# Optimization experiments

Measured on AMD Instinct MI355X. Metric: run time of the kernel, lower is better.

The kernel has to match this reference:

```python
import jax, jax.numpy as jnp
import numpy as np

HID = 1024   # hidden_dim
H = 16       # num_head
D = 64       # head_dim
W = 64       # window_size (one-sided attention radius)


def setup_inputs() -> dict:
    key = jax.random.key(0)
    ks = jax.random.split(key, 10)
    B, S = 2, 4096
    s = 0.02
    X = jax.random.normal(ks[0], (B, S, HID), jnp.float32)
    mask = jnp.ones((B, S), jnp.float32)
    Wq = jax.random.normal(ks[1], (HID, H * D), jnp.float32) * s
    bq = jnp.zeros((H * D,), jnp.float32)
    Wk = jax.random.normal(ks[2], (HID, H * D), jnp.float32) * s
    bk = jnp.zeros((H * D,), jnp.float32)
    Wv = jax.random.normal(ks[3], (HID, H * D), jnp.float32) * s
    bv = jnp.zeros((H * D,), jnp.float32)
    Wo = jax.random.normal(ks[4], (H * D, HID), jnp.float32) * s
    bo = jnp.zeros((HID,), jnp.float32)
    return dict(X=X, mask=mask, Wq=Wq, bq=bq, Wk=Wk, bk=bk, Wv=Wv, bv=bv, Wo=Wo, bo=bo)


def _chunk3(T, nC):
    # T: [B,H,S,D] -> [B,H,nC,3W,D]: for chunk c, keys of chunks c-1, c, c+1 (zero-padded at ends)
    B, Hh, S, Dd = T.shape
    Tp = jnp.pad(T, ((0, 0), (0, 0), (W, W), (0, 0))).reshape(B, Hh, nC + 2, W, Dd)
    return jnp.concatenate([Tp[:, :, :-2], Tp[:, :, 1:-1], Tp[:, :, 2:]], axis=3)


def reference(X, mask, Wq, bq, Wk, bk, Wv, bv, Wo, bo):
    B, S0, _ = X.shape
    pad = W - S0 % W  # matches torch: always >= 1 (full window if divisible)
    Xp = jnp.pad(X, ((0, 0), (0, pad), (0, 0)))
    mp = jnp.pad(mask, ((0, 0), (0, pad)))  # padded keys masked out
    S = S0 + pad
    nC = S // W

    def proj(Wm, b):
        return (Xp @ Wm + b).reshape(B, S, H, D).transpose(0, 2, 1, 3)  # [B,H,S,D]

    Q, K, V = proj(Wq, bq), proj(Wk, bk), proj(Wv, bv)
    Qc = Q.reshape(B, H, nC, W, D)
    K3 = _chunk3(K, nC)
    V3 = _chunk3(V, nC)

    # banded scores: query i attends keys j with |i - j| <= W
    scores = jnp.einsum('bhcqd,bhckd->bhcqk', Qc, K3) / jnp.asarray(np.sqrt(D), jnp.float32)
    qi = jnp.arange(W)[:, None]
    kj = jnp.arange(3 * W)[None, :]
    band = (kj >= qi) & (kj <= qi + 2 * W)  # [W, 3W]
    m3 = jnp.pad(mp, ((0, 0), (W, W))).reshape(B, nC + 2, W)
    m3 = jnp.concatenate([m3[:, :-2], m3[:, 1:-1], m3[:, 2:]], axis=2)  # [B,nC,3W]
    valid = band[None, None, None, :, :] & (m3[:, None, :, None, :] > 0)
    scores = jnp.where(valid, scores, -1e9)
    A = jax.nn.softmax(scores, axis=-1)
    ctx = jnp.einsum('bhcqk,bhckd->bhcqd', A, V3).reshape(B, H, S, D)
    out = ctx.transpose(0, 2, 1, 3).reshape(B, S, H * D) @ Wo + bo
    return out[:, :S0]
```

## Files before the change

kernel.cpp:

```cpp
#include <hip/hip_runtime.h>

typedef unsigned short u16;
typedef unsigned int u32;
typedef __bf16 bf16x8 __attribute__((ext_vector_type(8)));
typedef u16 u16x8 __attribute__((ext_vector_type(8)));
typedef float floatx4 __attribute__((ext_vector_type(4)));

#define MFMA16(a, b, c) __builtin_amdgcn_mfma_f32_16x16x32_bf16((a), (b), (c), 0, 0, 0)

#define B_ 2
#define S0 4096
#define NH 16
#define HD 64
#define HID 1024

__device__ __forceinline__ float bf2f(u16 u) {
  union { u32 i; float f; } x; x.i = ((u32)u) << 16; return x.f;
}
__device__ __forceinline__ u16 f2bf(float f) {
  union { float f; u32 i; } x; x.f = f;
  u32 r = x.i + 0x7FFFu + ((x.i >> 16) & 1u);
  return (u16)(r >> 16);
}

__device__ __forceinline__ void glds16(const u16* g, u16* l) {
  __builtin_amdgcn_global_load_lds(
      (const __attribute__((address_space(1))) u32*)g,
      (__attribute__((address_space(3))) u32*)l, 16, 0, 0);
}

__global__ __launch_bounds__(256) void prep(
    const float* __restrict__ X, const float* __restrict__ mask,
    const float* __restrict__ Wq, const float* __restrict__ bq,
    const float* __restrict__ Wk, const float* __restrict__ bk,
    const float* __restrict__ Wv, const float* __restrict__ bv,
    const float* __restrict__ Wo, const float* __restrict__ bo,
    u16* __restrict__ cX, u16* __restrict__ cmask, u16* __restrict__ cb,
    u16* __restrict__ WqkvT, u16* __restrict__ WoT) {
  __shared__ u16 tile[64][66];
  int bid = blockIdx.x;
  if (bid < 4096) {
    int i = (bid * 256 + threadIdx.x) * 8;
    u16x8 v;
#pragma unroll
    for (int j = 0; j < 8; j++) v[j] = f2bf(X[i + j]);
    *(u16x8*)(cX + i) = v;
  } else if (bid < 4144) {
    int tid = (bid - 4096) * 256 + threadIdx.x;
    if (tid < B_ * S0) {
      cmask[tid] = f2bf(mask[tid]);
    } else {
      int j = tid - B_ * S0;
      int seg = j >> 10, idx = j & 1023;
      const float* src = (seg == 0) ? bq : (seg == 1) ? bk : (seg == 2) ? bv : bo;
      cb[seg * 1024 + idx] = f2bf(src[idx]);
    }
  } else {
    int idx = bid - 4144;
    int mat = idx >> 8;
    const float* src = (mat == 0) ? Wq : (mat == 1) ? Wk : (mat == 2) ? Wv : Wo;
    u16* dst = (mat < 3) ? (WqkvT + (size_t)mat * HID * HID) : WoT;
    int t0 = ((idx >> 4) & 15) * 64;
    int c0 = (idx & 15) * 64;
    int tx = threadIdx.x & 63, ty = threadIdx.x >> 6;
#pragma unroll
    for (int i = 0; i < 16; i++) {
      int r = i * 4 + ty;
      tile[r][tx] = f2bf(src[(size_t)(t0 + r) * HID + c0 + tx]);
    }
    __syncthreads();
#pragma unroll
    for (int i = 0; i < 16; i++) {
      int r = i * 4 + ty;
      dst[(size_t)(c0 + r) * HID + t0 + tx] = tile[tx][r];
    }
  }
}

template <int BN, int MODE>
__global__ __launch_bounds__(256) void gemm_bf16_tn(
    const u16* __restrict__ A, const u16* __restrict__ Bt,
    const u16* __restrict__ cb, void* __restrict__ outp, int K) {
  constexpr int NT = BN / 32;
  __shared__ alignas(16) u16 sA[128 * 64];
  __shared__ alignas(16) u16 sB[BN * 64];
  int t = threadIdx.x;
  int wave = t >> 6, lane = t & 63;
  int wm = wave >> 1, wn = wave & 1;
  int quad = lane >> 4, l16 = lane & 15;
  int tile_m = blockIdx.x * 128;
  int tile_n = blockIdx.y * BN;

  floatx4 acc[4][NT] = {};

  int row_l = lane >> 3;
  int col_l = ((lane & 7) ^ row_l) * 8;
  const u16* Ag = A + (size_t)(tile_m + wave * 8 + row_l) * K + col_l;
  const u16* Bg = Bt + (size_t)(tile_n + wave * 8 + row_l) * K + col_l;
  u16* lA = sA + wave * 8 * 64;
  u16* lB = sB + wave * 8 * 64;

  for (int k0 = 0; k0 < K; k0 += 64) {
    __syncthreads();
#pragma unroll
    for (int r = 0; r < 4; r++)
      glds16(Ag + (size_t)(r * 32) * K + k0, lA + r * 2048);
#pragma unroll
    for (int r = 0; r < BN / 32; r++)
      glds16(Bg + (size_t)(r * 32) * K + k0, lB + r * 2048);
    __syncthreads();

#pragma unroll
    for (int ks = 0; ks < 2; ks++) {
      bf16x8 af[4], bfr[NT];
#pragma unroll
      for (int mt = 0; mt < 4; mt++) {
        int row = wm * 64 + mt * 16 + l16;
        int p = (ks * 4 + quad) ^ (row & 7);
        af[mt] = *(const bf16x8*)(sA + row * 64 + p * 8);
      }
#pragma unroll
      for (int nt = 0; nt < NT; nt++) {
        int row = wn * (BN / 2) + nt * 16 + l16;
        int p = (ks * 4 + quad) ^ (row & 7);
        bfr[nt] = *(const bf16x8*)(sB + row * 64 + p * 8);
      }
#pragma unroll
      for (int mt = 0; mt < 4; mt++)
#pragma unroll
        for (int nt = 0; nt < NT; nt++)
          acc[mt][nt] = MFMA16(af[mt], bfr[nt], acc[mt][nt]);
    }
  }

  if (MODE == 0) {
    u16* op = (u16*)outp;
#pragma unroll
    for (int mt = 0; mt < 4; mt++) {
      int row0 = tile_m + wm * 64 + mt * 16 + quad * 4;
      int bb = row0 >> 12;
      int sbase = row0 & (S0 - 1);
#pragma unroll
      for (int nt = 0; nt < NT; nt++) {
        int col = tile_n + wn * (BN / 2) + nt * 16 + l16;
        int p = col >> 10;
        int rem = col & 1023;
        float bias = bf2f(cb[p * 1024 + rem]);
        int hh = rem >> 6, dd = rem & 63;
        u16* dp = op + ((size_t)(((p * 2 + bb) * NH + hh)) * S0 + sbase) * HD + dd;
#pragma unroll
        for (int r = 0; r < 4; r++)
          dp[(size_t)r * HD] = f2bf(acc[mt][nt][r] + bias);
      }
    }
  } else {
    float* op = (float*)outp;
#pragma unroll
    for (int mt = 0; mt < 4; mt++) {
      int row0 = tile_m + wm * 64 + mt * 16 + quad * 4;
#pragma unroll
      for (int nt = 0; nt < NT; nt++) {
        int col = tile_n + wn * (BN / 2) + nt * 16 + l16;
        float bias = bf2f(cb[3 * 1024 + col]);
        float* dp = op + (size_t)row0 * HID + col;
#pragma unroll
        for (int r = 0; r < 4; r++)
          dp[(size_t)r * HID] = acc[mt][nt][r] + bias;
      }
    }
  }
}

__global__ __launch_bounds__(256) void attn_win(
    const u16* __restrict__ Q, const u16* __restrict__ Kp,
    const u16* __restrict__ Vp, const u16* __restrict__ cmask,
    u16* __restrict__ ctx) {
  __shared__ alignas(16) u16 sVt[64 * 208];
  __shared__ alignas(16) u16 sP[4 * 16 * 200];
  __shared__ u16 sMk[208];

  int bid = blockIdx.x;
  int c = bid & 63;
  int h = (bid >> 6) & 15;
  int b = bid >> 10;
  int t = threadIdx.x;
  int wave = t >> 6, lane = t & 63;
  int quad = lane >> 4, l16 = lane & 15;
  int koff = wave * 16;

  const u16* Qb = Q + (size_t)(b * NH + h) * S0 * HD;
  const u16* Kb = Kp + (size_t)(b * NH + h) * S0 * HD;
  const u16* Vb = Vp + (size_t)(b * NH + h) * S0 * HD;
  int kbase = (c - 1) * 64;

#pragma unroll
  for (int i = 0; i < 7; i++) {
    int e = i * 256 + t;
    if (e < 1664) {
      int dg = e / 208;
      int slot = e - dg * 208;
      int key = kbase + slot;
      int kc = key < 0 ? 0 : (key > S0 - 1 ? S0 - 1 : key);
      u16x8 v = *(const u16x8*)(Vb + (size_t)kc * HD + dg * 8);
#pragma unroll
      for (int j = 0; j < 8; j++) sVt[(dg * 8 + j) * 208 + slot] = v[j];
    }
  }
  if (t < 208) {
    int j = kbase + t;
    sMk[t] = (j >= 0 && j < S0) ? cmask[(size_t)b * S0 + j] : (u16)0;
  }
  __syncthreads();

  floatx4 sc[10] = {};
  int qrow = c * 64 + wave * 16 + l16;
#pragma unroll
  for (int ks = 0; ks < 2; ks++) {
    bf16x8 aq = *(const bf16x8*)(Qb + (size_t)qrow * HD + ks * 32 + quad * 8);
#pragma unroll
    for (int nt = 0; nt < 10; nt++) {
      int key = kbase + koff + nt * 16 + l16;
      int kc = key < 0 ? 0 : (key > S0 - 1 ? S0 - 1 : key);
      bf16x8 bk = *(const bf16x8*)(Kb + (size_t)kc * HD + ks * 32 + quad * 8);
      sc[nt] = MFMA16(aq, bk, sc[nt]);
    }
  }

  int qrel_base = wave * 16 + quad * 4;
  u16* myP = sP + wave * 16 * 200;
  float kmask[10];
#pragma unroll
  for (int nt = 0; nt < 10; nt++) kmask[nt] = bf2f(sMk[koff + nt * 16 + l16]);

#pragma unroll
  for (int reg = 0; reg < 4; reg++) {
    int qrel = qrel_base + reg;
    float v[10];
    float m = -3e38f;
#pragma unroll
    for (int nt = 0; nt < 10; nt++) {
      int jr = koff + nt * 16 + l16 - 64;
      bool ok = (jr >= qrel - 64) && (jr <= qrel + 64) && (kmask[nt] > 0.f);
      float s = ok ? sc[nt][reg] * 0.125f : -1e30f;
      v[nt] = s;
      m = fmaxf(m, s);
    }
#pragma unroll
    for (int off = 1; off <= 8; off <<= 1) m = fmaxf(m, __shfl_xor(m, off));
    float sum = 0.f;
#pragma unroll
    for (int nt = 0; nt < 10; nt++) {
      float p = __expf(v[nt] - m);
      v[nt] = p;
      sum += p;
    }
#pragma unroll
    for (int off = 1; off <= 8; off <<= 1) sum += __shfl_xor(sum, off);
    float inv = 1.0f / sum;
#pragma unroll
    for (int nt = 0; nt < 10; nt++)
      myP[(quad * 4 + reg) * 200 + nt * 16 + l16] = f2bf(v[nt] * inv);
  }
  __syncthreads();

  floatx4 oc[4] = {};
#pragma unroll
  for (int ks = 0; ks < 5; ks++) {
    bf16x8 ap = *(const bf16x8*)(myP + l16 * 200 + ks * 32 + quad * 8);
#pragma unroll
    for (int nt = 0; nt < 4; nt++) {
      bf16x8 bv =
          *(const bf16x8*)(sVt + (nt * 16 + l16) * 208 + koff + ks * 32 + quad * 8);
      oc[nt] = MFMA16(ap, bv, oc[nt]);
    }
  }

  int srow = c * 64 + wave * 16 + quad * 4;
#pragma unroll
  for (int nt = 0; nt < 4; nt++) {
    u16* dp = ctx + (size_t)(b * S0 + srow) * HID + h * HD + nt * 16 + l16;
#pragma unroll
    for (int reg = 0; reg < 4; reg++)
      dp[(size_t)reg * HID] = f2bf(oc[nt][reg]);
  }
}

extern "C" void kernel_launch(void* const* d_in, const int* in_sizes, int n_in,
                              void* d_out, int out_size, void* d_ws, size_t ws_size,
                              hipStream_t stream) {
  const float* X = (const float*)d_in[0];
  const float* mask = (const float*)d_in[1];
  const float* Wq = (const float*)d_in[2];
  const float* bq = (const float*)d_in[3];
  const float* Wk = (const float*)d_in[4];
  const float* bk = (const float*)d_in[5];
  const float* Wv = (const float*)d_in[6];
  const float* bv = (const float*)d_in[7];
  const float* Wo = (const float*)d_in[8];
  const float* bo = (const float*)d_in[9];
  char* ws = (char*)d_ws;

  const size_t MB = 1048576;
  u16* cmask = (u16*)(ws + 256);
  u16* cb = (u16*)(ws + 256 + 16384);
  u16* cX = (u16*)(ws + 1 * MB);
  u16* WqkvT = (u16*)(ws + 17 * MB);
  u16* WoT = (u16*)(ws + 23 * MB);
  u16* QKV = (u16*)(ws + 25 * MB);
  u16* CTX = cX;

  const size_t per_qkv = (size_t)B_ * NH * S0 * HD;

  prep<<<4096 + 48 + 1024, 256, 0, stream>>>(X, mask, Wq, bq, Wk, bk, Wv, bv,
                                             Wo, bo, cX, cmask, cb, WqkvT, WoT);
  gemm_bf16_tn<96, 0><<<dim3(64, 32), 256, 0, stream>>>(cX, WqkvT, cb, QKV, HID);
  attn_win<<<dim3(B_ * NH * 64), 256, 0, stream>>>(QKV, QKV + per_qkv,
                                                   QKV + 2 * per_qkv, cmask, CTX);
  gemm_bf16_tn<128, 1><<<dim3(64, 8), 256, 0, stream>>>(CTX, WoT, cb, d_out, HID);
}
```

Baseline: 230.8 us.

## Stage K tiles in LDS via direct loads and overlap V fetch with scores

The windowed attention kernel now copies the 208-key K window into shared memory with direct global-to-LDS loads and an XOR swizzle, instead of each lane reading K rows from global memory for every MFMA. V is loaded into registers while QK scores are computed, then transposed into the same shared buffer after the softmax. Each wave also drops one of its 10 key tiles because that tile always lies outside the band, and the unused P column is zero-filled. This cuts redundant global traffic and latency, but it adds an extra barrier and more register pressure from holding V in registers.

```diff
diff --git a/kernel.cpp b/kernel.cpp
--- a/kernel.cpp
+++ b/kernel.cpp
@@ -175,7 +175,7 @@
     const u16* __restrict__ Q, const u16* __restrict__ Kp,
     const u16* __restrict__ Vp, const u16* __restrict__ cmask,
     u16* __restrict__ ctx) {
-  __shared__ alignas(16) u16 sVt[64 * 208];
+  __shared__ alignas(16) u16 buf0[208 * 64];
   __shared__ alignas(16) u16 sP[4 * 16 * 200];
   __shared__ u16 sMk[208];
 
@@ -193,6 +193,38 @@
   const u16* Vb = Vp + (size_t)(b * NH + h) * S0 * HD;
   int kbase = (c - 1) * 64;
 
+  int rrow = lane >> 3;
+  int csrc = ((lane & 7) ^ rrow) * 8;
+#pragma unroll
+  for (int p = 0; p < 7; p++) {
+    int sl0 = p * 32 + wave * 8;
+    if (sl0 < 208) {
+      int key = kbase + sl0 + rrow;
+      int kc = key < 0 ? 0 : (key > S0 - 1 ? S0 - 1 : key);
+      glds16(Kb + (size_t)kc * HD + csrc, buf0 + sl0 * 64);
+    }
+  }
+  if (t < 208) {
+    int j = kbase + t;
+    sMk[t] = (j >= 0 && j < S0) ? cmask[(size_t)b * S0 + j] : (u16)0;
+  }
+  __syncthreads();
+
+  floatx4 sc[9] = {};
+  int qrow = c * 64 + wave * 16 + l16;
+#pragma unroll
+  for (int ks = 0; ks < 2; ks++) {
+    bf16x8 aq = *(const bf16x8*)(Qb + (size_t)qrow * HD + ks * 32 + quad * 8);
+#pragma unroll
+    for (int nt = 0; nt < 9; nt++) {
+      int slot = koff + nt * 16 + l16;
+      int pch = ((ks * 4 + quad) ^ (l16 & 7)) * 8;
+      bf16x8 bk = *(const bf16x8*)(buf0 + slot * 64 + pch);
+      sc[nt] = MFMA16(aq, bk, sc[nt]);
+    }
+  }
+
+  u16x8 vreg[7];
 #pragma unroll
   for (int i = 0; i < 7; i++) {
     int e = i * 256 + t;
@@ -201,46 +233,25 @@
       int slot = e - dg * 208;
       int key = kbase + slot;
       int kc = key < 0 ? 0 : (key > S0 - 1 ? S0 - 1 : key);
-      u16x8 v = *(const u16x8*)(Vb + (size_t)kc * HD + dg * 8);
-#pragma unroll
-      for (int j = 0; j < 8; j++) sVt[(dg * 8 + j) * 208 + slot] = v[j];
-    }
-  }
-  if (t < 208) {
-    int j = kbase + t;
-    sMk[t] = (j >= 0 && j < S0) ? cmask[(size_t)b * S0 + j] : (u16)0;
-  }
-  __syncthreads();
-
-  floatx4 sc[10] = {};
-  int qrow = c * 64 + wave * 16 + l16;
-#pragma unroll
-  for (int ks = 0; ks < 2; ks++) {
-    bf16x8 aq = *(const bf16x8*)(Qb + (size_t)qrow * HD + ks * 32 + quad * 8);
-#pragma unroll
-    for (int nt = 0; nt < 10; nt++) {
-      int key = kbase + koff + nt * 16 + l16;
-      int kc = key < 0 ? 0 : (key > S0 - 1 ? S0 - 1 : key);
-      bf16x8 bk = *(const bf16x8*)(Kb + (size_t)kc * HD + ks * 32 + quad * 8);
-      sc[nt] = MFMA16(aq, bk, sc[nt]);
+      vreg[i] = *(const u16x8*)(Vb + (size_t)kc * HD + dg * 8);
     }
   }
 
   int qrel_base = wave * 16 + quad * 4;
   u16* myP = sP + wave * 16 * 200;
-  float kmask[10];
-#pragma unroll
-  for (int nt = 0; nt < 10; nt++) kmask[nt] = bf2f(sMk[koff + nt * 16 + l16]);
+  float kmask[9];
+#pragma unroll
+  for (int nt = 0; nt < 9; nt++) kmask[nt] = bf2f(sMk[koff + nt * 16 + l16]);
 
 #pragma unroll
   for (int reg = 0; reg < 4; reg++) {
     int qrel = qrel_base + reg;
-    float v[10];
+    float v[9];
     float m = -3e38f;
 #pragma unroll
-    for (int nt = 0; nt < 10; nt++) {
-      int jr = koff + nt * 16 + l16 - 64;
-      bool ok = (jr >= qrel - 64) && (jr <= qrel + 64) && (kmask[nt] > 0.f);
+    for (int nt = 0; nt < 9; nt++) {
+      int slot = koff + nt * 16 + l16;
+      bool ok = (slot >= qrel) && (slot <= qrel + 128) && (kmask[nt] > 0.f);
       float s = ok ? sc[nt][reg] * 0.125f : -1e30f;
       v[nt] = s;
       m = fmaxf(m, s);
@@ -249,7 +260,7 @@
     for (int off = 1; off <= 8; off <<= 1) m = fmaxf(m, __shfl_xor(m, off));
     float sum = 0.f;
 #pragma unroll
-    for (int nt = 0; nt < 10; nt++) {
+    for (int nt = 0; nt < 9; nt++) {
       float p = __expf(v[nt] - m);
       v[nt] = p;
       sum += p;
@@ -257,9 +268,23 @@
 #pragma unroll
     for (int off = 1; off <= 8; off <<= 1) sum += __shfl_xor(sum, off);
     float inv = 1.0f / sum;
-#pragma unroll
-    for (int nt = 0; nt < 10; nt++)
-      myP[(quad * 4 + reg) * 200 + nt * 16 + l16] = f2bf(v[nt] * inv);
+    int prow = (quad * 4 + reg) * 200;
+#pragma unroll
+    for (int nt = 0; nt < 9; nt++)
+      myP[prow + nt * 16 + l16] = f2bf(v[nt] * inv);
+    myP[prow + 144 + l16] = 0;
+  }
+  __syncthreads();
+
+#pragma unroll
+  for (int i = 0; i < 7; i++) {
+    int e = i * 256 + t;
+    if (e < 1664) {
+      int dg = e / 208;
+      int slot = e - dg * 208;
+#pragma unroll
+      for (int j = 0; j < 8; j++) buf0[(dg * 8 + j) * 208 + slot] = vreg[i][j];
+    }
   }
   __syncthreads();
 
@@ -270,7 +295,7 @@
 #pragma unroll
     for (int nt = 0; nt < 4; nt++) {
       bf16x8 bv =
-          *(const bf16x8*)(sVt + (nt * 16 + l16) * 208 + koff + ks * 32 + quad * 8);
+          *(const bf16x8*)(buf0 + (nt * 16 + l16) * 208 + koff + ks * 32 + quad * 8);
       oc[nt] = MFMA16(ap, bv, oc[nt]);
     }
   }
```

Result: no change. 227.0 us (-1.7%).
